# Optimization experiments

Hardware: AMD Instinct MI355X
Metric: run time of the kernel (lower is better)

Reference implementation:

```python
import jax, jax.numpy as jnp
import numpy as np

V, E, H, L = 32000, 512, 1024, 2
B, T, S = 16, 128, 128
NEG = -1.0e9


def setup_inputs() -> dict:
    key = jax.random.key(0)
    ks = jax.random.split(key, 16)
    sc = 0.02
    inp = {
        "y_in": jax.random.randint(ks[0], (B, T), 0, V),
        "h0": jnp.zeros((L, B, H), jnp.float32),
        "c0": jnp.zeros((L, B, H), jnp.float32),
        "enc_out": jax.random.normal(ks[1], (B, S, H), jnp.float32),
        "enc_mask": jnp.ones((B, S), dtype=bool),
        # embedding (padding_idx=0 row zeroed, as nn.Embedding does)
        "embed": (jax.random.normal(ks[2], (V, E), jnp.float32) * sc).at[0].set(0.0),
        # LSTM layer 0 (input E) and layer 1 (input H); gate order i,f,g,o
        "W_ih0": jax.random.normal(ks[3], (4 * H, E), jnp.float32) * sc,
        "W_hh0": jax.random.normal(ks[4], (4 * H, H), jnp.float32) * sc,
        "b_ih0": jax.random.normal(ks[5], (4 * H,), jnp.float32) * sc,
        "b_hh0": jax.random.normal(ks[6], (4 * H,), jnp.float32) * sc,
        "W_ih1": jax.random.normal(ks[7], (4 * H, H), jnp.float32) * sc,
        "W_hh1": jax.random.normal(ks[8], (4 * H, H), jnp.float32) * sc,
        "b_ih1": jax.random.normal(ks[9], (4 * H,), jnp.float32) * sc,
        "b_hh1": jax.random.normal(ks[10], (4 * H,), jnp.float32) * sc,
        "fc_W": jax.random.normal(ks[11], (H, 2 * H), jnp.float32) * sc,
        "fc_b": jax.random.normal(ks[12], (H,), jnp.float32) * sc,
        "out_W": jax.random.normal(ks[13], (V, H), jnp.float32) * sc,
        "out_b": jax.random.normal(ks[14], (V,), jnp.float32) * sc,
    }
    return inp


def _lstm_layer(x, W_ih, W_hh, b_ih, b_hh, h0, c0):
    # x: [B,T,in] -> outputs [B,T,H]. PyTorch LSTM cell, gates i,f,g,o.
    xg = jnp.einsum("bti,gi->btg", x, W_ih) + b_ih  # precompute input gates

    def step(carry, xg_t):
        h, c = carry
        g = xg_t + h @ W_hh.T + b_hh
        i, f, gg, o = jnp.split(g, 4, axis=-1)
        c = jax.nn.sigmoid(f) * c + jax.nn.sigmoid(i) * jnp.tanh(gg)
        h = jax.nn.sigmoid(o) * jnp.tanh(c)
        return (h, c), h

    _, hs = jax.lax.scan(step, (h0, c0), jnp.swapaxes(xg, 0, 1))
    return jnp.swapaxes(hs, 0, 1)


def reference(y_in, h0, c0, enc_out, enc_mask, embed,
              W_ih0, W_hh0, b_ih0, b_hh0, W_ih1, W_hh1, b_ih1, b_hh1,
              fc_W, fc_b, out_W, out_b):
    # Teacher forcing: step t consumes y_in[:, t-1]; all T input tokens = y_in.
    emb = embed[y_in]  # [B,T,E]
    out = _lstm_layer(emb, W_ih0, W_hh0, b_ih0, b_hh0, h0[0], c0[0])
    out = _lstm_layer(out, W_ih1, W_hh1, b_ih1, b_hh1, h0[1], c0[1])  # [B,T,H]
    # Dot attention, batched over all decode steps t
    scores = jnp.einsum("bth,bsh->bts", out, enc_out)
    scores = jnp.where(enc_mask[:, None, :], scores, NEG)
    attn = jax.nn.softmax(scores, axis=-1)
    ctx = jnp.einsum("bts,bsh->bth", attn, enc_out)
    cat = jnp.concatenate([out, ctx], axis=-1)  # [B,T,2H]
    h_t = jnp.tanh(cat @ fc_W.T + fc_b)
    logits = h_t @ out_W.T + out_b  # [B,T,V]
    return logits
```

## Files before the change

### kernel.cpp

```cpp
#include <hip/hip_runtime.h>
#include <cstdint>
#include <cstddef>

#define TT 128
#define NBATCH 16
#define HH 1024
#define G4 4096

typedef __attribute__((ext_vector_type(8))) short bf16x8;
typedef __attribute__((ext_vector_type(4))) float f32x4;

__global__ __launch_bounds__(256) void embed_kernel(const int* __restrict__ y,
    const float* __restrict__ embed, float* __restrict__ emb) {
  int idx = blockIdx.x * 256 + threadIdx.x;
  int n = idx >> 7, c = idx & 127;
  int tok = y[n];
  reinterpret_cast<float4*>(emb)[idx] =
      reinterpret_cast<const float4*>(embed)[(size_t)tok * 128 + c];
}

__device__ __forceinline__ unsigned pkhi(float x, float y) {
  return (__float_as_uint(x) >> 16) | (__float_as_uint(y) & 0xFFFF0000u);
}
__device__ __forceinline__ float bfres(float x) {
  return x - __uint_as_float(__float_as_uint(x) & 0xFFFF0000u);
}

__global__ __launch_bounds__(256, 2) void gemm_mfma(
    const float* __restrict__ A, const float* __restrict__ W,
    const float* __restrict__ b1, const float* __restrict__ b2,
    float* __restrict__ C, int M, int N, int K, int act) {
  __shared__ short Ah[128][40];
  __shared__ short Al[128][40];
  __shared__ short Wh[128][40];
  __shared__ short Wl[128][40];

  const int tid = threadIdx.x;
  const int m0 = blockIdx.y * 128, n0 = blockIdx.x * 128;
  const int sr = tid >> 1;
  const int kh = tid & 1;
  const int lane = tid & 63;
  const int wv = tid >> 6;
  const int wr = wv >> 1, wc = wv & 1;
  const int lr = lane & 15;
  const int kg = lane >> 4;

  const float* Ap = A + (size_t)(m0 + sr) * K + kh * 16;
  const float* Wp = W + (size_t)(n0 + sr) * K + kh * 16;

  f32x4 zero = {0.f, 0.f, 0.f, 0.f};
  f32x4 acc[4][4];
#pragma unroll
  for (int m = 0; m < 4; ++m)
#pragma unroll
    for (int n = 0; n < 4; ++n) acc[m][n] = zero;

  float4 qa[4], qw[4];
#pragma unroll
  for (int i = 0; i < 4; ++i) {
    qa[i] = *reinterpret_cast<const float4*>(Ap + i * 4);
    qw[i] = *reinterpret_cast<const float4*>(Wp + i * 4);
  }

  for (int k0 = 0; k0 < K; k0 += 32) {
    {
      unsigned ha[8], la[8], hw[8], lw[8];
#pragma unroll
      for (int i = 0; i < 4; ++i) {
        ha[2 * i]     = pkhi(qa[i].x, qa[i].y);
        ha[2 * i + 1] = pkhi(qa[i].z, qa[i].w);
        la[2 * i]     = pkhi(bfres(qa[i].x), bfres(qa[i].y));
        la[2 * i + 1] = pkhi(bfres(qa[i].z), bfres(qa[i].w));
        hw[2 * i]     = pkhi(qw[i].x, qw[i].y);
        hw[2 * i + 1] = pkhi(qw[i].z, qw[i].w);
        lw[2 * i]     = pkhi(bfres(qw[i].x), bfres(qw[i].y));
        lw[2 * i + 1] = pkhi(bfres(qw[i].z), bfres(qw[i].w));
      }
      *reinterpret_cast<uint4*>(&Ah[sr][kh * 16])     = make_uint4(ha[0], ha[1], ha[2], ha[3]);
      *reinterpret_cast<uint4*>(&Ah[sr][kh * 16 + 8]) = make_uint4(ha[4], ha[5], ha[6], ha[7]);
      *reinterpret_cast<uint4*>(&Al[sr][kh * 16])     = make_uint4(la[0], la[1], la[2], la[3]);
      *reinterpret_cast<uint4*>(&Al[sr][kh * 16 + 8]) = make_uint4(la[4], la[5], la[6], la[7]);
      *reinterpret_cast<uint4*>(&Wh[sr][kh * 16])     = make_uint4(hw[0], hw[1], hw[2], hw[3]);
      *reinterpret_cast<uint4*>(&Wh[sr][kh * 16 + 8]) = make_uint4(hw[4], hw[5], hw[6], hw[7]);
      *reinterpret_cast<uint4*>(&Wl[sr][kh * 16])     = make_uint4(lw[0], lw[1], lw[2], lw[3]);
      *reinterpret_cast<uint4*>(&Wl[sr][kh * 16 + 8]) = make_uint4(lw[4], lw[5], lw[6], lw[7]);
    }
    __syncthreads();

    if (k0 + 32 < K) {
#pragma unroll
      for (int i = 0; i < 4; ++i) {
        qa[i] = *reinterpret_cast<const float4*>(Ap + k0 + 32 + i * 4);
        qw[i] = *reinterpret_cast<const float4*>(Wp + k0 + 32 + i * 4);
      }
    }

    bf16x8 fah[4], fal[4], fbh[4], fbl[4];
#pragma unroll
    for (int m = 0; m < 4; ++m) {
      fah[m] = *reinterpret_cast<const bf16x8*>(&Ah[wr * 64 + m * 16 + lr][kg * 8]);
      fal[m] = *reinterpret_cast<const bf16x8*>(&Al[wr * 64 + m * 16 + lr][kg * 8]);
      fbh[m] = *reinterpret_cast<const bf16x8*>(&Wh[wc * 64 + m * 16 + lr][kg * 8]);
      fbl[m] = *reinterpret_cast<const bf16x8*>(&Wl[wc * 64 + m * 16 + lr][kg * 8]);
    }

#pragma unroll
    for (int m = 0; m < 4; ++m)
#pragma unroll
      for (int n = 0; n < 4; ++n)
        acc[m][n] = __builtin_amdgcn_mfma_f32_16x16x32_bf16(fah[m], fbh[n], acc[m][n], 0, 0, 0);
#pragma unroll
    for (int m = 0; m < 4; ++m)
#pragma unroll
      for (int n = 0; n < 4; ++n)
        acc[m][n] = __builtin_amdgcn_mfma_f32_16x16x32_bf16(fah[m], fbl[n], acc[m][n], 0, 0, 0);
#pragma unroll
    for (int m = 0; m < 4; ++m)
#pragma unroll
      for (int n = 0; n < 4; ++n)
        acc[m][n] = __builtin_amdgcn_mfma_f32_16x16x32_bf16(fal[m], fbh[n], acc[m][n], 0, 0, 0);
    __syncthreads();
  }

#pragma unroll
  for (int m = 0; m < 4; ++m) {
    int grow = m0 + wr * 64 + m * 16 + kg * 4;
#pragma unroll
    for (int n = 0; n < 4; ++n) {
      int gcol = n0 + wc * 64 + n * 16 + lr;
      float bias = b1[gcol] + (b2 ? b2[gcol] : 0.f);
#pragma unroll
      for (int rr = 0; rr < 4; ++rr) {
        float v = acc[m][n][rr] + bias;
        if (act) v = tanhf(v);
        C[(size_t)(grow + rr) * N + gcol] = v;
      }
    }
  }
}

__device__ __forceinline__ void grid_barrier(unsigned* bar) {
  __syncthreads();
  if (threadIdx.x == 0) {
    unsigned* gen  = bar + 32;
    unsigned* leaf = bar + 64 + (blockIdx.x >> 4) * 32;
    unsigned g = __hip_atomic_load(gen, __ATOMIC_RELAXED, __HIP_MEMORY_SCOPE_AGENT);
    unsigned a = __hip_atomic_fetch_add(leaf, 1u, __ATOMIC_ACQ_REL, __HIP_MEMORY_SCOPE_AGENT);
    if (a == 15u) {
      __hip_atomic_store(leaf, 0u, __ATOMIC_RELAXED, __HIP_MEMORY_SCOPE_AGENT);
      unsigned r = __hip_atomic_fetch_add(bar, 1u, __ATOMIC_ACQ_REL, __HIP_MEMORY_SCOPE_AGENT);
      if (r == 15u) {
        __hip_atomic_store(bar, 0u, __ATOMIC_RELAXED, __HIP_MEMORY_SCOPE_AGENT);
        __hip_atomic_fetch_add(gen, 1u, __ATOMIC_RELEASE, __HIP_MEMORY_SCOPE_AGENT);
      }
    }
    while (__hip_atomic_load(gen, __ATOMIC_RELAXED, __HIP_MEMORY_SCOPE_AGENT) == g) {
      __builtin_amdgcn_s_sleep(2);
    }
    (void)__hip_atomic_load(gen, __ATOMIC_ACQUIRE, __HIP_MEMORY_SCOPE_AGENT);
  }
  __syncthreads();
}

__global__ __launch_bounds__(256) void lstm_kernel(
    const float* __restrict__ xg,
    const float* __restrict__ W_hh,
    const float* __restrict__ h0,
    const float* __restrict__ c0,
    float* __restrict__ hbuf0,
    float* __restrict__ hbuf1,
    float* __restrict__ hs,
    unsigned* __restrict__ bar) {
  __shared__ float4 lds_h[16 * 256];
  float* lds_g = reinterpret_cast<float*>(lds_h);

  const int tid = threadIdx.x;
  const int bid = blockIdx.x;
  const int r = tid >> 4;
  const int ks = tid & 15;
  const int gate = r >> 2, jj = r & 3;
  const int grow = gate * HH + bid * 4 + jj;

  float4 wreg[16];
#pragma unroll
  for (int m = 0; m < 16; ++m)
    wreg[m] = *reinterpret_cast<const float4*>(W_hh + (size_t)grow * HH + ks * 4 + 64 * m);

  float c_reg = 0.f;
  if (tid < 64) {
    int b = tid & 15, jl = tid >> 4;
    int j = bid * 4 + jl;
    c_reg = c0[b * HH + j];
    hbuf0[b * HH + j] = h0[b * HH + j];
  }
  grid_barrier(bar);

  float* cur = hbuf0;
  float* nxt = hbuf1;
  for (int t = 0; t < TT; ++t) {
    float xgv = xg[(size_t)(ks * TT + t) * G4 + grow];
    const float4* hg4 = reinterpret_cast<const float4*>(cur);
#pragma unroll
    for (int i = 0; i < 16; ++i) {
      int idx = i * 256 + tid;
      lds_h[idx] = hg4[idx];
    }
    __syncthreads();
    float acc[16];
#pragma unroll
    for (int b = 0; b < 16; ++b) {
      float fa = 0.f;
#pragma unroll
      for (int m = 0; m < 16; ++m) {
        float4 hv = lds_h[b * 256 + m * 16 + ks];
        fa += wreg[m].x * hv.x + wreg[m].y * hv.y + wreg[m].z * hv.z + wreg[m].w * hv.w;
      }
      acc[b] = fa;
    }
#pragma unroll
    for (int b = 0; b < 16; ++b) {
      float v = acc[b];
      v += __shfl_xor(v, 1);
      v += __shfl_xor(v, 2);
      v += __shfl_xor(v, 4);
      v += __shfl_xor(v, 8);
      acc[b] = v;
    }
    float gv = acc[0];
#pragma unroll
    for (int b = 1; b < 16; ++b) if (ks == b) gv = acc[b];
    gv += xgv;
    __syncthreads();
    lds_g[r * 17 + ks] = gv;
    __syncthreads();
    if (tid < 64) {
      int b = tid & 15, jl = tid >> 4;
      float gi = lds_g[(0 * 4 + jl) * 17 + b];
      float gf = lds_g[(1 * 4 + jl) * 17 + b];
      float gg = lds_g[(2 * 4 + jl) * 17 + b];
      float go = lds_g[(3 * 4 + jl) * 17 + b];
      float si = 1.f / (1.f + expf(-gi));
      float sf = 1.f / (1.f + expf(-gf));
      float so = 1.f / (1.f + expf(-go));
      c_reg = sf * c_reg + si * tanhf(gg);
      float hv = so * tanhf(c_reg);
      int j = bid * 4 + jl;
      nxt[b * HH + j] = hv;
      hs[(size_t)(b * TT + t) * HH + j] = hv;
    }
    grid_barrier(bar);
    float* tmp = cur; cur = nxt; nxt = tmp;
  }
}

__global__ __launch_bounds__(256) void attn_kernel(
    const float* __restrict__ hs1, const float* __restrict__ enc,
    const int* __restrict__ mask, float* __restrict__ cat) {
  __shared__ float4 q4[256];
  __shared__ float sc[128];
  __shared__ float red[8];
  const int tid = threadIdx.x;
  const int n = blockIdx.x;
  const int b = n >> 7;

  float4 qv = reinterpret_cast<const float4*>(hs1)[(size_t)n * 256 + tid];
  q4[tid] = qv;
  reinterpret_cast<float4*>(cat)[(size_t)n * 512 + tid] = qv;
  __syncthreads();

  const int s = tid >> 1, half = tid & 1;
  const float4* e4 = reinterpret_cast<const float4*>(enc) + ((size_t)(b * 128 + s)) * 256 + half * 128;
  const float4* qq = q4 + half * 128;
  float p = 0.f;
#pragma unroll 8
  for (int k = 0; k < 128; ++k) {
    float4 ev = e4[k]; float4 qk = qq[k];
    p += ev.x * qk.x + ev.y * qk.y + ev.z * qk.z + ev.w * qk.w;
  }
  p += __shfl_xor(p, 1);
  if (half == 0) sc[s] = (mask[b * 128 + s] != 0) ? p : -1.0e9f;
  __syncthreads();

  const int lane = tid & 63;
  float v = (tid < 128) ? sc[tid] : -3.4e38f;
#pragma unroll
  for (int off = 32; off; off >>= 1) v = fmaxf(v, __shfl_xor(v, off));
  if (tid < 128 && lane == 0) red[tid >> 6] = v;
  __syncthreads();
  float mx = fmaxf(red[0], red[1]);
  float e = (tid < 128) ? expf(sc[tid] - mx) : 0.f;
  float sum = e;
#pragma unroll
  for (int off = 32; off; off >>= 1) sum += __shfl_xor(sum, off);
  if (lane == 0) red[4 + (tid >> 6)] = sum;
  __syncthreads();
  float tot = red[4] + red[5] + red[6] + red[7];
  if (tid < 128) sc[tid] = e / tot;
  __syncthreads();

  float4 accv = {0.f, 0.f, 0.f, 0.f};
  const float4* eb = reinterpret_cast<const float4*>(enc) + (size_t)b * 128 * 256;
#pragma unroll 4
  for (int ss = 0; ss < 128; ++ss) {
    float a = sc[ss];
    float4 ev = eb[(size_t)ss * 256 + tid];
    accv.x += a * ev.x; accv.y += a * ev.y; accv.z += a * ev.z; accv.w += a * ev.w;
  }
  reinterpret_cast<float4*>(cat)[(size_t)n * 512 + 256 + tid] = accv;
}

extern "C" void kernel_launch(void* const* d_in, const int* in_sizes, int n_in,
                              void* d_out, int out_size, void* d_ws, size_t ws_size,
                              hipStream_t stream) {
  const int* y_in = (const int*)d_in[0];
  const float* h0 = (const float*)d_in[1];
  const float* c0 = (const float*)d_in[2];
  const float* enc = (const float*)d_in[3];
  const int* mask = (const int*)d_in[4];
  const float* embed = (const float*)d_in[5];
  const float* W_ih0 = (const float*)d_in[6];
  const float* W_hh0 = (const float*)d_in[7];
  const float* b_ih0 = (const float*)d_in[8];
  const float* b_hh0 = (const float*)d_in[9];
  const float* W_ih1 = (const float*)d_in[10];
  const float* W_hh1 = (const float*)d_in[11];
  const float* b_ih1 = (const float*)d_in[12];
  const float* b_hh1 = (const float*)d_in[13];
  const float* fc_W = (const float*)d_in[14];
  const float* fc_b = (const float*)d_in[15];
  const float* out_W = (const float*)d_in[16];
  const float* out_b = (const float*)d_in[17];
  float* out = (float*)d_out;

  float* ws = (float*)d_ws;
  float* emb   = ws;
  float* xg    = emb + 1048576;
  float* hs0   = xg + 8388608;
  float* hs1   = hs0 + 2097152;
  float* hglob0 = hs1 + 2097152;
  float* hglob1 = hglob0 + 16384;
  unsigned* bar = (unsigned*)(hglob1 + 16384);
  float* cat = xg;
  float* h_t = xg + 4194304;

  hipMemsetAsync(bar, 0, 1024 * sizeof(unsigned), stream);
  embed_kernel<<<1024, 256, 0, stream>>>(y_in, embed, emb);
  gemm_mfma<<<dim3(32, 16), 256, 0, stream>>>(emb, W_ih0, b_ih0, b_hh0, xg, 2048, 4096, 512, 0);
  lstm_kernel<<<256, 256, 0, stream>>>(xg, W_hh0, h0, c0, hglob0, hglob1, hs0, bar);
  gemm_mfma<<<dim3(32, 16), 256, 0, stream>>>(hs0, W_ih1, b_ih1, b_hh1, xg, 2048, 4096, 1024, 0);
  lstm_kernel<<<256, 256, 0, stream>>>(xg, W_hh1, h0 + 16384, c0 + 16384, hglob0, hglob1, hs1, bar);
  attn_kernel<<<2048, 256, 0, stream>>>(hs1, enc, mask, cat);
  gemm_mfma<<<dim3(8, 16), 256, 0, stream>>>(cat, fc_W, fc_b, nullptr, h_t, 2048, 1024, 2048, 1);
  gemm_mfma<<<dim3(250, 16), 256, 0, stream>>>(h_t, out_W, out_b, nullptr, out, 2048, 32000, 1024, 0);
}
```

Measured before the change: 5.912 ms.

## Use monotonic relaxed-atomic grid barrier with coherent h exchange in LSTM

Replaces the reset-based generation barrier with monotonically increasing counters (target 16*n), so counter resets and acquire/release fences are no longer needed. The hidden-state exchange buffers are now written and read with relaxed agent-scope atomics, so data is fetched coherently without full cache invalidation or writeback fences. Each LSTM layer gets its own barrier region. The aim is lower per-timestep barrier latency across 128 steps, at the cost of relying on vmcnt waits and atomic memory semantics for correctness.

```diff
diff --git a/kernel.cpp b/kernel.cpp
--- a/kernel.cpp
+++ b/kernel.cpp
@@ -139,26 +139,24 @@
   }
 }
 
-__device__ __forceinline__ void grid_barrier(unsigned* bar) {
+__device__ __forceinline__ void grid_barrier(unsigned* bar, unsigned n) {
   __syncthreads();
   if (threadIdx.x == 0) {
     unsigned* gen  = bar + 32;
     unsigned* leaf = bar + 64 + (blockIdx.x >> 4) * 32;
-    unsigned g = __hip_atomic_load(gen, __ATOMIC_RELAXED, __HIP_MEMORY_SCOPE_AGENT);
-    unsigned a = __hip_atomic_fetch_add(leaf, 1u, __ATOMIC_ACQ_REL, __HIP_MEMORY_SCOPE_AGENT);
-    if (a == 15u) {
-      __hip_atomic_store(leaf, 0u, __ATOMIC_RELAXED, __HIP_MEMORY_SCOPE_AGENT);
-      unsigned r = __hip_atomic_fetch_add(bar, 1u, __ATOMIC_ACQ_REL, __HIP_MEMORY_SCOPE_AGENT);
-      if (r == 15u) {
-        __hip_atomic_store(bar, 0u, __ATOMIC_RELAXED, __HIP_MEMORY_SCOPE_AGENT);
-        __hip_atomic_fetch_add(gen, 1u, __ATOMIC_RELEASE, __HIP_MEMORY_SCOPE_AGENT);
-      }
-    }
-    while (__hip_atomic_load(gen, __ATOMIC_RELAXED, __HIP_MEMORY_SCOPE_AGENT) == g) {
+    asm volatile("s_waitcnt vmcnt(0)" ::: "memory");
+    unsigned a = __hip_atomic_fetch_add(leaf, 1u, __ATOMIC_RELAXED, __HIP_MEMORY_SCOPE_AGENT);
+    if (a == 16u * n - 1u) {
+      unsigned r = __hip_atomic_fetch_add(bar, 1u, __ATOMIC_RELAXED, __HIP_MEMORY_SCOPE_AGENT);
+      if (r == 16u * n - 1u) {
+        __hip_atomic_fetch_add(gen, 1u, __ATOMIC_RELAXED, __HIP_MEMORY_SCOPE_AGENT);
+      }
+    }
+    while (__hip_atomic_load(gen, __ATOMIC_RELAXED, __HIP_MEMORY_SCOPE_AGENT) < n) {
       __builtin_amdgcn_s_sleep(2);
     }
-    (void)__hip_atomic_load(gen, __ATOMIC_ACQUIRE, __HIP_MEMORY_SCOPE_AGENT);
-  }
+  }
+  asm volatile("" ::: "memory");
   __syncthreads();
 }
 
@@ -191,19 +189,22 @@
     int b = tid & 15, jl = tid >> 4;
     int j = bid * 4 + jl;
     c_reg = c0[b * HH + j];
-    hbuf0[b * HH + j] = h0[b * HH + j];
-  }
-  grid_barrier(bar);
+    __hip_atomic_store(reinterpret_cast<unsigned*>(&hbuf0[b * HH + j]),
+                       __float_as_uint(h0[b * HH + j]),
+                       __ATOMIC_RELAXED, __HIP_MEMORY_SCOPE_AGENT);
+  }
+  grid_barrier(bar, 1);
 
   float* cur = hbuf0;
   float* nxt = hbuf1;
   for (int t = 0; t < TT; ++t) {
     float xgv = xg[(size_t)(ks * TT + t) * G4 + grow];
-    const float4* hg4 = reinterpret_cast<const float4*>(cur);
-#pragma unroll
-    for (int i = 0; i < 16; ++i) {
+    const unsigned long long* hg8 = reinterpret_cast<const unsigned long long*>(cur);
+    unsigned long long* lds8 = reinterpret_cast<unsigned long long*>(lds_h);
+#pragma unroll
+    for (int i = 0; i < 32; ++i) {
       int idx = i * 256 + tid;
-      lds_h[idx] = hg4[idx];
+      lds8[idx] = __hip_atomic_load(hg8 + idx, __ATOMIC_RELAXED, __HIP_MEMORY_SCOPE_AGENT);
     }
     __syncthreads();
     float acc[16];
@@ -245,10 +246,12 @@
       c_reg = sf * c_reg + si * tanhf(gg);
       float hv = so * tanhf(c_reg);
       int j = bid * 4 + jl;
-      nxt[b * HH + j] = hv;
+      __hip_atomic_store(reinterpret_cast<unsigned*>(&nxt[b * HH + j]),
+                         __float_as_uint(hv),
+                         __ATOMIC_RELAXED, __HIP_MEMORY_SCOPE_AGENT);
       hs[(size_t)(b * TT + t) * HH + j] = hv;
     }
-    grid_barrier(bar);
+    grid_barrier(bar, (unsigned)t + 2u);
     float* tmp = cur; cur = nxt; nxt = tmp;
   }
 }
@@ -339,16 +342,17 @@
   float* hs1   = hs0 + 2097152;
   float* hglob0 = hs1 + 2097152;
   float* hglob1 = hglob0 + 16384;
-  unsigned* bar = (unsigned*)(hglob1 + 16384);
+  unsigned* bar0 = (unsigned*)(hglob1 + 16384);
+  unsigned* bar1 = bar0 + 1024;
   float* cat = xg;
   float* h_t = xg + 4194304;
 
-  hipMemsetAsync(bar, 0, 1024 * sizeof(unsigned), stream);
+  hipMemsetAsync(bar0, 0, 2048 * sizeof(unsigned), stream);
   embed_kernel<<<1024, 256, 0, stream>>>(y_in, embed, emb);
   gemm_mfma<<<dim3(32, 16), 256, 0, stream>>>(emb, W_ih0, b_ih0, b_hh0, xg, 2048, 4096, 512, 0);
-  lstm_kernel<<<256, 256, 0, stream>>>(xg, W_hh0, h0, c0, hglob0, hglob1, hs0, bar);
+  lstm_kernel<<<256, 256, 0, stream>>>(xg, W_hh0, h0, c0, hglob0, hglob1, hs0, bar0);
   gemm_mfma<<<dim3(32, 16), 256, 0, stream>>>(hs0, W_ih1, b_ih1, b_hh1, xg, 2048, 4096, 1024, 0);
-  lstm_kernel<<<256, 256, 0, stream>>>(xg, W_hh1, h0 + 16384, c0 + 16384, hglob0, hglob1, hs1, bar);
+  lstm_kernel<<<256, 256, 0, stream>>>(xg, W_hh1, h0 + 16384, c0 + 16384, hglob0, hglob1, hs1, bar1);
   attn_kernel<<<2048, 256, 0, stream>>>(hs1, enc, mask, cat);
   gemm_mfma<<<dim3(8, 16), 256, 0, stream>>>(cat, fc_W, fc_b, nullptr, h_t, 2048, 1024, 2048, 1);
   gemm_mfma<<<dim3(250, 16), 256, 0, stream>>>(h_t, out_W, out_b, nullptr, out, 2048, 32000, 1024, 0);
```

Result: slower. 6.742 ms (+14.0%).
